# Performance work log

Hardware: AMD Instinct MI355X
Metric: run time of the kernel (lower is better)

The kernel has to match this reference:

```python
import jax, jax.numpy as jnp
import numpy as np

B, D, K = 32, 64, 26      # batch, n_objects, per-object feature dim
QST = 256                  # question embedding size
G = [512, 512, 512, 512, 512, 512, 28]  # g_layers (last = n_answers)
IN = 2 * K                 # in_size = concat(x_i, x_j)
AGG = 4                    # aggregation + question injection position


def setup_inputs() -> dict:
    key = jax.random.key(0)
    ks = jax.random.split(key, 2 + 2 * len(G))
    inp = {
        "x": jax.random.normal(ks[0], (B, D, K), jnp.float32),
        "qst": jax.random.normal(ks[1], (B, QST), jnp.float32),
    }
    prev = IN
    for i, g in enumerate(G):
        d_in = prev + (QST if i == AGG else 0)
        inp[f"W{i}"] = jax.random.normal(ks[2 + 2 * i], (g, d_in), jnp.float32) * (1.0 / np.sqrt(d_in))
        inp[f"b{i}"] = jnp.zeros((g,), jnp.float32)
        prev = g
    return inp


def reference(x, qst, W0, b0, W1, b1, W2, b2, W3, b3, W4, b4, W5, b5, W6, b6):
    b, d, k = x.shape
    # all ordered pairs: x_full[b, p, q] = [x[b, q], x[b, p]]  (matches torch repeat/cat order)
    xi = jnp.broadcast_to(x[:, None, :, :], (b, d, d, k))
    xj = jnp.broadcast_to(x[:, :, None, :], (b, d, d, k))
    h = jnp.concatenate([xi, xj], axis=-1).reshape(b * d * d, 2 * k)
    Ws = [W0, W1, W2, W3, W4, W5, W6]
    bs = [b0, b1, b2, b3, b4, b5, b6]
    n = len(Ws)
    for i in range(n):
        if i == AGG:
            # sum-aggregation over all d^2 pairs, then question injection
            h = h.reshape(b, d * d, h.shape[-1]).sum(axis=1)  # [b, g]
            h = jnp.concatenate([h, qst], axis=1)             # [b, g+qst]
        h = h @ Ws[i].T + bs[i]
        if i != n - 1:
            h = jax.nn.relu(h)
    return jax.nn.log_softmax(h, axis=1)
```

## Files before the change

### kernel.cpp

```cpp
#include <hip/hip_runtime.h>
#include <math.h>


typedef __attribute__((ext_vector_type(8))) short bf16x8;
typedef __attribute__((ext_vector_type(4))) float f32x4;
typedef __attribute__((ext_vector_type(4))) unsigned int u32x4;

__device__ __forceinline__ unsigned short f2bf(float f) {
    union { float f; unsigned u; } x; x.f = f;
    unsigned r = x.u + 0x7fffu + ((x.u >> 16) & 1u);
    return (unsigned short)(r >> 16);
}

#define NPV_WP   98304
#define NPV_W0P  4096
#define NPV_W4   98304
#define NPV_W5   65536
#define NPV_TOTAL (NPV_WP + NPV_W0P + NPV_W4 + NPV_W5)
__global__ void k_prep(const float* __restrict__ W1, const float* __restrict__ W2,
                       const float* __restrict__ W3, const float* __restrict__ W0,
                       const float* __restrict__ W4, const float* __restrict__ W5,
                       unsigned short* __restrict__ Wp,
                       unsigned short* __restrict__ W0p,
                       float* __restrict__ W4v,
                       float* __restrict__ W5v)
{
    int f = blockIdx.x * 256 + threadIdx.x;
    if (f < NPV_WP) {
        int l = f >> 15, r = f & 32767;
        int n = r >> 6, kq = r & 63;
        const float* W = (l == 0) ? W1 : (l == 1) ? W2 : W3;
        const float* src = W + n * 512 + kq * 8;
        int s = kq >> 2, q4 = kq & 3;
        int wv = n >> 6, jj = (n >> 4) & 3, i16 = n & 15;
        int lane = q4 * 16 + i16;
        unsigned w[4];
        #pragma unroll
        for (int h = 0; h < 4; ++h)
            w[h] = (unsigned)f2bf(src[h * 2]) | ((unsigned)f2bf(src[h * 2 + 1]) << 16);
        *(u32x4*)(Wp + (size_t)l * 262144 + ((((wv * 16 + s) * 4 + jj) * 64 + lane) << 3))
            = (u32x4){w[0], w[1], w[2], w[3]};
    } else if (f < NPV_WP + NPV_W0P) {
        int g = f - NPV_WP;
        int n = g >> 3, kq = g & 7;
        int s = kq >> 2, q4 = kq & 3;
        int wv = n >> 6, jj = (n >> 4) & 3, i16 = n & 15;
        int lane = q4 * 16 + i16;
        unsigned w[4];
        #pragma unroll
        for (int h = 0; h < 4; ++h) {
            int k0 = kq * 8 + h * 2, k1 = k0 + 1;
            float f0 = (k0 < 52) ? W0[n * 52 + k0] : 0.f;
            float f1 = (k1 < 52) ? W0[n * 52 + k1] : 0.f;
            w[h] = (unsigned)f2bf(f0) | ((unsigned)f2bf(f1) << 16);
        }
        *(u32x4*)(W0p + ((((wv * 2 + s) * 4 + jj) * 64 + lane) << 3))
            = (u32x4){w[0], w[1], w[2], w[3]};
    } else if (f < NPV_WP + NPV_W0P + NPV_W4) {
        int g = f - (NPV_WP + NPV_W0P);
        int o = g / 192, kb = g % 192;
        float4 w = *(const float4*)(W4 + (size_t)o * 768 + kb * 4);
        *(float4*)(W4v + (size_t)kb * 2048 + o * 4) = w;
    } else {
        int g = f - (NPV_WP + NPV_W0P + NPV_W4);
        int o = g >> 7, kb = g & 127;
        float4 w = *(const float4*)(W5 + (size_t)o * 512 + kb * 4);
        *(float4*)(W5v + (size_t)kb * 2048 + o * 4) = w;
    }
}

__device__ __forceinline__ void store_h(const f32x4 (&acc)[4][4], const float* __restrict__ bl,
                                        unsigned short* hsm, int wave, int i16, int q4, int lane)
{
    char* base = (char*)hsm;
    #pragma unroll
    for (int j = 0; j < 4; ++j) {
        int col = (wave * 4 + j) * 16 + i16;
        int g = col >> 3;
        int e = g & 7;
        float bb = bl[col];
        char* colbase = base + g * 1024 + ((col & 7) << 1);
        #pragma unroll
        for (int mt = 0; mt < 4; ++mt) {
            #pragma unroll
            for (int r = 0; r < 4; ++r) {
                int row = mt * 16 + q4 * 4 + r;
                float v = fmaxf(acc[mt][j][r] + bb, 0.f);
                int vi = __float_as_int(v);
                int swi = __builtin_amdgcn_update_dpp(0, vi, 0xB1, 0xF, 0xF, true);
                if ((lane & 1) == 0) {
                    unsigned pk;
                    asm("v_cvt_pk_bf16_f32 %0, %1, %2" : "=v"(pk) : "v"(vi), "v"(swi));
                    int slot = row ^ e;
                    *(unsigned*)(colbase + slot * 16) = pk;
                }
            }
        }
    }
}

#define CLUSTER(AV0, AV1, AV2, AV3, BV, JJ)                                              \
    __builtin_amdgcn_s_setprio(1);                                                      \
    acc[0][JJ] = __builtin_amdgcn_mfma_f32_16x16x32_bf16(AV0, BV, acc[0][JJ], 0, 0, 0); \
    acc[1][JJ] = __builtin_amdgcn_mfma_f32_16x16x32_bf16(AV1, BV, acc[1][JJ], 0, 0, 0); \
    acc[2][JJ] = __builtin_amdgcn_mfma_f32_16x16x32_bf16(AV2, BV, acc[2][JJ], 0, 0, 0); \
    acc[3][JJ] = __builtin_amdgcn_mfma_f32_16x16x32_bf16(AV3, BV, acc[3][JJ], 0, 0, 0); \
    __builtin_amdgcn_s_setprio(0);                                                      \
    __builtin_amdgcn_sched_barrier(0);

__global__ __launch_bounds__(512, 2) void k_fused(
    const float* __restrict__ x,
    const unsigned short* __restrict__ Wp,
    const unsigned short* __restrict__ W0p,
    const float* __restrict__ b0, const float* __restrict__ b1,
    const float* __restrict__ b2, const float* __restrict__ b3,
    float* __restrict__ P)
{
    __shared__ __align__(16) unsigned short hsm[64 * 512];
    __shared__ __align__(16) unsigned short xs[8 * 64 * 8];
    int t = threadIdx.x;
    int blk = blockIdx.x;
    int b = blk >> 6, p = blk & 63;

    {
        int row = t >> 3, gr = t & 7;
        const float* xq = x + (size_t)(b * 64 + row) * 26;
        const float* xp = x + (size_t)(b * 64 + p) * 26;
        unsigned w[4];
        #pragma unroll
        for (int h = 0; h < 4; ++h) {
            int k0 = gr * 8 + h * 2;
            int k1 = k0 + 1;
            float f0 = (k0 < 26) ? xq[k0] : (k0 < 52 ? xp[k0 - 26] : 0.f);
            float f1 = (k1 < 26) ? xq[k1] : (k1 < 52 ? xp[k1 - 26] : 0.f);
            w[h] = (unsigned)f2bf(f0) | ((unsigned)f2bf(f1) << 16);
        }
        *(u32x4*)((char*)xs + gr * 1024 + ((row ^ gr) << 4)) = (u32x4){w[0], w[1], w[2], w[3]};
    }

    int wave = t >> 6, lane = t & 63;
    int i16 = lane & 15, q4 = lane >> 4;

    f32x4 acc[4][4];

    __syncthreads();

    {
        #pragma unroll
        for (int mt = 0; mt < 4; ++mt)
            #pragma unroll
            for (int j = 0; j < 4; ++j)
                acc[mt][j] = (f32x4){0.f, 0.f, 0.f, 0.f};
        const unsigned short* Bb0 = W0p + wave * 4096 + lane * 8;
        const char* xb = (const char*)xs;
        #pragma unroll
        for (int s = 0; s < 2; ++s) {
            bf16x8 bfr[4];
            #pragma unroll
            for (int j = 0; j < 4; ++j)
                bfr[j] = *(const bf16x8*)(Bb0 + s * 2048 + j * 512);
            int g = s * 4 + q4;
            const char* A0 = xb + g * 1024 + ((i16 ^ g) << 4);
            #pragma unroll
            for (int mt = 0; mt < 4; ++mt) {
                bf16x8 a = *(const bf16x8*)(A0 + mt * 256);
                #pragma unroll
                for (int j = 0; j < 4; ++j)
                    acc[mt][j] = __builtin_amdgcn_mfma_f32_16x16x32_bf16(a, bfr[j], acc[mt][j], 0, 0, 0);
            }
        }
        store_h(acc, b0, hsm, wave, i16, q4, lane);
    }

    int A_even = (q4 << 10) + ((i16 ^ q4) << 4);
    const char* hbe = (const char*)hsm + A_even;
    const char* hbo = (const char*)hsm + 4096 + (A_even ^ 64);

    #pragma unroll 1
    for (int l = 0; l < 3; ++l) {
        const float* bl = (l == 0) ? b1 : (l == 1) ? b2 : b3;
        const unsigned short* Bb = Wp + (size_t)l * 262144 + wave * 32768 + lane * 8;

        bf16x8 X0 = *(const bf16x8*)(Bb);
        bf16x8 X1 = *(const bf16x8*)(Bb + 512);
        bf16x8 X2 = *(const bf16x8*)(Bb + 1024);
        bf16x8 X3 = *(const bf16x8*)(Bb + 1536);
        bf16x8 Y0 = *(const bf16x8*)(Bb + 2048);
        bf16x8 Y1 = *(const bf16x8*)(Bb + 2560);
        bf16x8 Y2 = *(const bf16x8*)(Bb + 3072);
        bf16x8 Y3 = *(const bf16x8*)(Bb + 3584);

        __syncthreads();

        #pragma unroll
        for (int mt = 0; mt < 4; ++mt)
            #pragma unroll
            for (int j = 0; j < 4; ++j)
                acc[mt][j] = (f32x4){0.f, 0.f, 0.f, 0.f};

        bf16x8 aE0 = *(const bf16x8*)(hbe);
        bf16x8 aE1 = *(const bf16x8*)(hbe + 256);
        bf16x8 aE2 = *(const bf16x8*)(hbe + 512);
        bf16x8 aE3 = *(const bf16x8*)(hbe + 768);
        bf16x8 aO0, aO1, aO2, aO3;

        #pragma unroll 1
        for (int s = 0; s < 16; s += 2) {
            {
                const unsigned short* BX = Bb + ((s + 2 < 16) ? (s + 2) : 14) * 2048;
                const char* po = hbo + (s << 12);
                CLUSTER(aE0, aE1, aE2, aE3, X0, 0)
                X0 = *(const bf16x8*)(BX);
                aO0 = *(const bf16x8*)(po);
                aO1 = *(const bf16x8*)(po + 256);
                CLUSTER(aE0, aE1, aE2, aE3, X1, 1)
                X1 = *(const bf16x8*)(BX + 512);
                aO2 = *(const bf16x8*)(po + 512);
                aO3 = *(const bf16x8*)(po + 768);
                CLUSTER(aE0, aE1, aE2, aE3, X2, 2)
                X2 = *(const bf16x8*)(BX + 1024);
                CLUSTER(aE0, aE1, aE2, aE3, X3, 3)
                X3 = *(const bf16x8*)(BX + 1536);
            }
            {
                const unsigned short* BY = Bb + ((s + 3 < 16) ? (s + 3) : 15) * 2048;
                const char* pe = hbe + ((s + 2 < 16 ? s + 2 : 14) << 12);
                CLUSTER(aO0, aO1, aO2, aO3, Y0, 0)
                Y0 = *(const bf16x8*)(BY);
                aE0 = *(const bf16x8*)(pe);
                aE1 = *(const bf16x8*)(pe + 256);
                CLUSTER(aO0, aO1, aO2, aO3, Y1, 1)
                Y1 = *(const bf16x8*)(BY + 512);
                aE2 = *(const bf16x8*)(pe + 512);
                aE3 = *(const bf16x8*)(pe + 768);
                CLUSTER(aO0, aO1, aO2, aO3, Y2, 2)
                Y2 = *(const bf16x8*)(BY + 1024);
                CLUSTER(aO0, aO1, aO2, aO3, Y3, 3)
                Y3 = *(const bf16x8*)(BY + 1536);
            }
        }
        __syncthreads();

        if (l < 2) {
            store_h(acc, bl, hsm, wave, i16, q4, lane);
        } else {
            #pragma unroll
            for (int j = 0; j < 4; ++j) {
                int col = (wave * 4 + j) * 16 + i16;
                float bb = bl[col];
                float sum = 0.f;
                #pragma unroll
                for (int mt = 0; mt < 4; ++mt)
                    #pragma unroll
                    for (int r = 0; r < 4; ++r)
                        sum += fmaxf(acc[mt][j][r] + bb, 0.f);
                sum += __shfl_xor(sum, 16);
                sum += __shfl_xor(sum, 32);
                if (q4 == 0) P[(size_t)blk * 512 + col] = sum;
            }
        }
    }
}

__global__ __launch_bounds__(1024) void k_tail(
    const float* __restrict__ P, const float* __restrict__ qst,
    const float* __restrict__ W4v, const float* __restrict__ b4,
    const float* __restrict__ W5v, const float* __restrict__ b5,
    const float* __restrict__ W6, const float* __restrict__ b6,
    float* __restrict__ out)
{
    int b = blockIdx.x, t = threadIdx.x;
    __shared__ __align__(16) float z[768];
    __shared__ __align__(16) float ps[1024];
    __shared__ __align__(16) float h4[512];
    __shared__ float h5[512];
    __shared__ float logits[28];
    __shared__ float red[2];

    if (t < 512) {
        float s = 0.f;
        const float* Pb = P + (size_t)b * 64 * 512 + t;
        #pragma unroll 8
        for (int c = 0; c < 64; ++c) s += Pb[c * 512];
        z[t] = s;
    } else if (t < 768) {
        z[t] = qst[b * 256 + (t - 512)];
    }
    __syncthreads();
    {
        int o = t & 511, hf = t >> 9;
        float acc = 0.f;
        const float4* Wv = (const float4*)W4v;
        const float4* z4 = (const float4*)z;
        #pragma unroll 4
        for (int kb = hf * 96; kb < hf * 96 + 96; ++kb) {
            float4 w = Wv[kb * 512 + o];
            float4 zz = z4[kb];
            acc = fmaf(w.x, zz.x, acc);
            acc = fmaf(w.y, zz.y, acc);
            acc = fmaf(w.z, zz.z, acc);
            acc = fmaf(w.w, zz.w, acc);
        }
        ps[t] = acc;
    }
    __syncthreads();
    if (t < 512) h4[t] = fmaxf(ps[t] + ps[t + 512] + b4[t], 0.f);
    __syncthreads();
    {
        int o = t & 511, hf = t >> 9;
        float acc = 0.f;
        const float4* Wv = (const float4*)W5v;
        const float4* h44 = (const float4*)h4;
        #pragma unroll 4
        for (int kb = hf * 64; kb < hf * 64 + 64; ++kb) {
            float4 w = Wv[kb * 512 + o];
            float4 hh = h44[kb];
            acc = fmaf(w.x, hh.x, acc);
            acc = fmaf(w.y, hh.y, acc);
            acc = fmaf(w.z, hh.z, acc);
            acc = fmaf(w.w, hh.w, acc);
        }
        ps[t] = acc;
    }
    __syncthreads();
    if (t < 512) h5[t] = fmaxf(ps[t] + ps[t + 512] + b5[t], 0.f);
    __syncthreads();
    {
        int o = t >> 5, c = t & 31;
        if (o < 28) {
            float acc = 0.f;
            for (int k = c; k < 512; k += 32) acc = fmaf(W6[o * 512 + k], h5[k], acc);
            acc += __shfl_xor(acc, 1);
            acc += __shfl_xor(acc, 2);
            acc += __shfl_xor(acc, 4);
            acc += __shfl_xor(acc, 8);
            acc += __shfl_xor(acc, 16);
            if (c == 0) logits[o] = acc + b6[o];
        }
    }
    __syncthreads();
    if (t == 0) {
        float mx = -1e30f;
        for (int cc = 0; cc < 28; ++cc) mx = fmaxf(mx, logits[cc]);
        float se = 0.f;
        for (int cc = 0; cc < 28; ++cc) se += expf(logits[cc] - mx);
        red[0] = mx; red[1] = logf(se);
    }
    __syncthreads();
    if (t < 28) out[b * 28 + t] = logits[t] - red[0] - red[1];
}

extern "C" void kernel_launch(void* const* d_in, const int* in_sizes, int n_in,
                              void* d_out, int out_size, void* d_ws, size_t ws_size,
                              hipStream_t stream)
{
    const float* x   = (const float*)d_in[0];
    const float* qst = (const float*)d_in[1];
    const float* W0  = (const float*)d_in[2];
    const float* b0  = (const float*)d_in[3];
    const float* W1  = (const float*)d_in[4];
    const float* b1  = (const float*)d_in[5];
    const float* W2  = (const float*)d_in[6];
    const float* b2  = (const float*)d_in[7];
    const float* W3  = (const float*)d_in[8];
    const float* b3  = (const float*)d_in[9];
    const float* W4  = (const float*)d_in[10];
    const float* b4  = (const float*)d_in[11];
    const float* W5  = (const float*)d_in[12];
    const float* b5  = (const float*)d_in[13];
    const float* W6  = (const float*)d_in[14];
    const float* b6  = (const float*)d_in[15];
    float* out = (float*)d_out;

    char* ws = (char*)d_ws;
    unsigned short* Wp  = (unsigned short*)(ws);
    unsigned short* W0p = (unsigned short*)(ws + 1572864);
    float*          W4v = (float*)(ws + 1638400);
    float*          W5v = (float*)(ws + 3211264);
    float*          P   = (float*)(ws + 4259840);

    k_prep <<<NPV_TOTAL / 256, 256, 0, stream>>>(W1, W2, W3, W0, W4, W5,
                                                 Wp, W0p, W4v, W5v);
    k_fused<<<2048, 512, 0, stream>>>(x, Wp, W0p, b0, b1, b2, b3, P);
    k_tail <<<32, 1024, 0, stream>>>(P, qst, W4v, b4, W5v, b5, W6, b6, out);
}
```

Before: 322.9 us.

## Double-buffer hidden activations in LDS and prefetch next layer weights early

Allocates two LDS buffers for hidden activations so each layer writes its output into the alternate buffer. This removes one block-wide barrier per layer. The first weight fragments of the next layer are loaded before storing activations, to overlap global loads with the epilogue. The cost is doubled LDS use per block, which likely cuts resident blocks per CU and so reduces latency hiding.

```diff
diff --git a/kernel.cpp b/kernel.cpp
--- a/kernel.cpp
+++ b/kernel.cpp
@@ -70,9 +70,9 @@
 }
 
 __device__ __forceinline__ void store_h(const f32x4 (&acc)[4][4], const float* __restrict__ bl,
-                                        unsigned short* hsm, int wave, int i16, int q4, int lane)
-{
-    char* base = (char*)hsm;
+                                        unsigned short* hbuf, int wave, int i16, int q4, int lane)
+{
+    char* base = (char*)hbuf;
     #pragma unroll
     for (int j = 0; j < 4; ++j) {
         int col = (wave * 4 + j) * 16 + i16;
@@ -116,7 +116,7 @@
     const float* __restrict__ b2, const float* __restrict__ b3,
     float* __restrict__ P)
 {
-    __shared__ __align__(16) unsigned short hsm[64 * 512];
+    __shared__ __align__(16) unsigned short hsm[2 * 64 * 512];
     __shared__ __align__(16) unsigned short xs[8 * 64 * 8];
     int t = threadIdx.x;
     int blk = blockIdx.x;
@@ -142,6 +142,9 @@
     int i16 = lane & 15, q4 = lane >> 4;
 
     f32x4 acc[4][4];
+    bf16x8 X0, X1, X2, X3, Y0, Y1, Y2, Y3;
+
+    const unsigned short* Bb0base = Wp + wave * 32768 + lane * 8;
 
     __syncthreads();
 
@@ -151,14 +154,14 @@
             #pragma unroll
             for (int j = 0; j < 4; ++j)
                 acc[mt][j] = (f32x4){0.f, 0.f, 0.f, 0.f};
-        const unsigned short* Bb0 = W0p + wave * 4096 + lane * 8;
+        const unsigned short* Bw0 = W0p + wave * 4096 + lane * 8;
         const char* xb = (const char*)xs;
         #pragma unroll
         for (int s = 0; s < 2; ++s) {
             bf16x8 bfr[4];
             #pragma unroll
             for (int j = 0; j < 4; ++j)
-                bfr[j] = *(const bf16x8*)(Bb0 + s * 2048 + j * 512);
+                bfr[j] = *(const bf16x8*)(Bw0 + s * 2048 + j * 512);
             int g = s * 4 + q4;
             const char* A0 = xb + g * 1024 + ((i16 ^ g) << 4);
             #pragma unroll
@@ -169,28 +172,28 @@
                     acc[mt][j] = __builtin_amdgcn_mfma_f32_16x16x32_bf16(a, bfr[j], acc[mt][j], 0, 0, 0);
             }
         }
+        X0 = *(const bf16x8*)(Bb0base);
+        X1 = *(const bf16x8*)(Bb0base + 512);
+        X2 = *(const bf16x8*)(Bb0base + 1024);
+        X3 = *(const bf16x8*)(Bb0base + 1536);
+        Y0 = *(const bf16x8*)(Bb0base + 2048);
+        Y1 = *(const bf16x8*)(Bb0base + 2560);
+        Y2 = *(const bf16x8*)(Bb0base + 3072);
+        Y3 = *(const bf16x8*)(Bb0base + 3584);
         store_h(acc, b0, hsm, wave, i16, q4, lane);
     }
+    __syncthreads();
 
     int A_even = (q4 << 10) + ((i16 ^ q4) << 4);
-    const char* hbe = (const char*)hsm + A_even;
-    const char* hbo = (const char*)hsm + 4096 + (A_even ^ 64);
+    int A_odd  = 4096 + (A_even ^ 64);
 
     #pragma unroll 1
     for (int l = 0; l < 3; ++l) {
         const float* bl = (l == 0) ? b1 : (l == 1) ? b2 : b3;
-        const unsigned short* Bb = Wp + (size_t)l * 262144 + wave * 32768 + lane * 8;
-
-        bf16x8 X0 = *(const bf16x8*)(Bb);
-        bf16x8 X1 = *(const bf16x8*)(Bb + 512);
-        bf16x8 X2 = *(const bf16x8*)(Bb + 1024);
-        bf16x8 X3 = *(const bf16x8*)(Bb + 1536);
-        bf16x8 Y0 = *(const bf16x8*)(Bb + 2048);
-        bf16x8 Y1 = *(const bf16x8*)(Bb + 2560);
-        bf16x8 Y2 = *(const bf16x8*)(Bb + 3072);
-        bf16x8 Y3 = *(const bf16x8*)(Bb + 3584);
-
-        __syncthreads();
+        const unsigned short* Bb = Bb0base + (size_t)l * 262144;
+        const char* hb = (const char*)hsm + (l & 1) * 65536;
+        const char* hbe = hb + A_even;
+        const char* hbo = hb + A_odd;
 
         #pragma unroll
         for (int mt = 0; mt < 4; ++mt)
@@ -239,10 +242,20 @@
                 Y3 = *(const bf16x8*)(BY + 1536);
             }
         }
-        __syncthreads();
 
         if (l < 2) {
-            store_h(acc, bl, hsm, wave, i16, q4, lane);
+            const unsigned short* Bn = Bb + 262144;
+            X0 = *(const bf16x8*)(Bn);
+            X1 = *(const bf16x8*)(Bn + 512);
+            X2 = *(const bf16x8*)(Bn + 1024);
+            X3 = *(const bf16x8*)(Bn + 1536);
+            Y0 = *(const bf16x8*)(Bn + 2048);
+            Y1 = *(const bf16x8*)(Bn + 2560);
+            Y2 = *(const bf16x8*)(Bn + 3072);
+            Y3 = *(const bf16x8*)(Bn + 3584);
+            store_h(acc, bl, (unsigned short*)((char*)hsm + ((l + 1) & 1) * 65536),
+                    wave, i16, q4, lane);
+            __syncthreads();
         } else {
             #pragma unroll
             for (int j = 0; j < 4; ++j) {
```

Result: no change. 322.1 us (-0.3%).
